# Kernel optimization log

Measured on AMD Instinct MI355X. Metric: run time of the kernel, lower is better.

Reference implementation:

```python
import jax, jax.numpy as jnp
import numpy as np

WL_W = 8   # weight quantization bits (args.wl_weight)
WL_A = 8   # activation quantization bits (args.wl_activate)
EPS = 1e-5


def _quant_ste(x, bits):
    """Symmetric per-tensor uniform quantization with straight-through estimator,
    emulating NeuroSim's wage-style weight/activation quantization in QConv2d."""
    n = float(2 ** (bits - 1) - 1)
    s = jnp.max(jnp.abs(x)) + 1e-12
    xq = jnp.round(x / s * n) / n * s
    return x + jax.lax.stop_gradient(xq - x)


def _qconv(x, w):
    # quantize input and weight, then 3x3 conv, stride 1, padding 1 (NCHW/OIHW)
    xq = _quant_ste(x, WL_A)
    wq = _quant_ste(w, WL_W)
    return jax.lax.conv_general_dilated(
        xq, wq, window_strides=(1, 1), padding=((1, 1), (1, 1)),
        dimension_numbers=('NCHW', 'OIHW', 'NCHW'))


def _bn(x, gamma, beta):
    # training-mode BatchNorm2d: batch statistics over (N, H, W)
    mean = jnp.mean(x, axis=(0, 2, 3), keepdims=True)
    var = jnp.var(x, axis=(0, 2, 3), keepdims=True)
    xn = (x - mean) * jax.lax.rsqrt(var + EPS)
    return xn * gamma[None, :, None, None] + beta[None, :, None, None]


def setup_inputs() -> dict:
    key = jax.random.key(0)
    ks = jax.random.split(key, 3)
    B, C, H, W = 32, 128, 56, 56
    return {
        'x': jax.random.normal(ks[0], (B, C, H, W), dtype=jnp.float32),
        'w1': jax.random.normal(ks[1], (C, C, 3, 3), dtype=jnp.float32) * 0.05,
        'gamma1': jnp.ones((C,), dtype=jnp.float32),
        'beta1': jnp.zeros((C,), dtype=jnp.float32),
        'w2': jax.random.normal(ks[2], (C, C, 3, 3), dtype=jnp.float32) * 0.05,
        'gamma2': jnp.ones((C,), dtype=jnp.float32),
        'beta2': jnp.zeros((C,), dtype=jnp.float32),
    }


def reference(x, w1, gamma1, beta1, w2, gamma2, beta2):
    identity = x  # no downsample
    out = _qconv(x, w1)
    out = _bn(out, gamma1, beta1)
    out = jax.nn.relu(out)
    out = _qconv(out, w2)
    out = _bn(out, gamma2, beta2)
    out = out + identity
    return jax.nn.relu(out)
```

## Files before the change

### kernel.cpp

```cpp
#include <hip/hip_runtime.h>

#define NB 32
#define C 128
#define H 56
#define W 56
#define HWSZ (H*W)
#define ELTS (NB*C*HWSZ)
#define NHW (NB*HWSZ)
#define HP 59
#define SLAB 8192
#define GCONVX 28
#define NBLK (GCONVX*NB)
#define PSTRIDE (C*NBLK)

typedef __attribute__((ext_vector_type(8))) short bf16x8;
typedef __attribute__((ext_vector_type(4))) short short4v;
typedef __attribute__((ext_vector_type(4))) float f32x4;
typedef __attribute__((ext_vector_type(4))) int i32x4;

#define SLOT_SX 0
#define SLOT_SW1 1
#define SLOT_SW2 2
#define SLOT_SA2 3
#define SUM1 8
#define SSQ1 136
#define MAXE1 264
#define MAXNEG1 392
#define SCALE1 520
#define SHIFT1 648
#define SUM2 776
#define SSQ2 904
#define MAXE2 1032
#define MAXNEG2 1160
#define SCALE2 1288
#define SHIFT2 1416

#define META_OFF 0ull
#define META_BYTES 8192ull
#define XQ_OFF 8192ull
#define XQ_BYTES ((unsigned long long)NB*HP*SLAB)
#define A2Q_OFF (XQ_OFF + XQ_BYTES)
#define Y1_OFF (A2Q_OFF + XQ_BYTES)
#define Y_BYTES ((unsigned long long)ELTS*2ull)
#define Y2_OFF (Y1_OFF + Y_BYTES)
#define W1Q_OFF (Y2_OFF + Y_BYTES)
#define WQ_BYTES (9ull*2*128*64)
#define W2Q_OFF (W1Q_OFF + WQ_BYTES)
#define PART_OFF (W2Q_OFF + WQ_BYTES)
#define PART_BYTES (4ull*PSTRIDE*4ull)

__device__ __forceinline__ short f2bf_rne(float f) {
    unsigned u = __float_as_uint(f);
    return (short)((u + 0x7FFFu + ((u >> 16) & 1u)) >> 16);
}
__device__ __forceinline__ float bf2f(short s) {
    return __uint_as_float(((unsigned)(unsigned short)s) << 16);
}

__global__ void absmax_kernel(const float* __restrict__ p, int n4, unsigned* __restrict__ slot) {
    __shared__ float red[256];
    float m = 0.f;
    int stride = gridDim.x * blockDim.x;
    for (int i = blockIdx.x * blockDim.x + threadIdx.x; i < n4; i += stride) {
        f32x4 v = ((const f32x4*)p)[i];
        m = fmaxf(m, fmaxf(fmaxf(fabsf(v.x), fabsf(v.y)), fmaxf(fabsf(v.z), fabsf(v.w))));
    }
    red[threadIdx.x] = m;
    __syncthreads();
    for (int s = 128; s > 0; s >>= 1) {
        if (threadIdx.x < s) red[threadIdx.x] = fmaxf(red[threadIdx.x], red[threadIdx.x + s]);
        __syncthreads();
    }
    if (threadIdx.x == 0) atomicMax(slot, __float_as_uint(red[0]));
}

__global__ void pad_zero_kernel(char* __restrict__ xq, char* __restrict__ a2q) {
    int hp = blockIdx.x;
    int n = blockIdx.y;
    char* base = (blockIdx.z ? a2q : xq) + ((size_t)n * HP + hp) * SLAB;
    int t = threadIdx.x;
    if (hp == 0 || hp >= 57) {
        f32x4 z = {0.f, 0.f, 0.f, 0.f};
        *(f32x4*)(base + t * 16) = z;
        *(f32x4*)(base + 4096 + t * 16) = z;
    } else {
        if (t < 32) *(int*)(base + t * 4) = 0;
        else        *(int*)(base + 7296 + (t - 32) * 4) = 0;
    }
}

__global__ void quant_w_kernel(const float* __restrict__ w, const float* __restrict__ meta,
                               int slot, char* __restrict__ wq) {
    int idx = blockIdx.x * 256 + threadIdx.x;
    int co = idx >> 7, ci = idx & 127;
    float qs = 127.f / (meta[slot] + 1e-12f);
    const float* src = w + ((size_t)(co * 128 + ci)) * 9;
    int cc = ci >> 6, cl = ci & 63;
    #pragma unroll
    for (int tap = 0; tap < 9; ++tap) {
        int q = (int)rintf(src[tap] * qs);
        wq[(((size_t)tap * 2 + cc) * 128 + co) * 64 + cl] = (char)q;
    }
}

__global__ void quant_x_kernel(const float* __restrict__ x, const float* __restrict__ meta,
                               char* __restrict__ xq) {
    __shared__ float tile[128][57];
    int h = blockIdx.x, n = blockIdx.y, t = threadIdx.x;
    int ci = t >> 1, seg = (t & 1) * 28;
    const float* row = x + (((size_t)(n * C + ci)) * H + h) * W + seg;
    #pragma unroll
    for (int j = 0; j < 28; j += 4) {
        f32x4 v = *(const f32x4*)(row + j);
        tile[ci][seg + j + 0] = v.x;
        tile[ci][seg + j + 1] = v.y;
        tile[ci][seg + j + 2] = v.z;
        tile[ci][seg + j + 3] = v.w;
    }
    __syncthreads();
    float qs = 127.f / (meta[SLOT_SX] + 1e-12f);
    int w = t & 63, cq = t >> 6;
    if (w < 56) {
        char* slab = xq + ((size_t)n * HP + (h + 1)) * SLAB;
        int wp = w + 1;
        #pragma unroll
        for (int c2 = 0; c2 < 2; ++c2) {
            union { char c[16]; i32x4 v; } u;
            #pragma unroll
            for (int j = 0; j < 16; ++j)
                u.c[j] = (char)(int)rintf(tile[cq * 32 + c2 * 16 + j][w] * qs);
            int L = wp * 128 + cq * 32 + c2 * 16;
            *(i32x4*)(slab + (L ^ ((wp & 7) << 4))) = u.v;
        }
    }
}

__global__ __launch_bounds__(256, 4) void conv_mfma_kernel(
        const char* __restrict__ xq, const char* __restrict__ wq,
        short* __restrict__ y, const float* __restrict__ meta,
        float* __restrict__ part, int slot_in, int slot_w) {
    __shared__ __align__(16) char lds[4 * SLAB + 512];
    const int n = blockIdx.y, h0 = blockIdx.x * 2;
    const int t = threadIdx.x, lane = t & 63;
    const int co0 = (t >> 6) * 32, l15 = lane & 15, lg = lane >> 4;

    const char* slabbase = xq + ((size_t)n * HP + h0) * SLAB;
    #pragma unroll
    for (int s = 0; s < 4; ++s) {
        #pragma unroll
        for (int i = 0; i < 2; ++i) {
            int off = (i * 256 + t) * 16;
            __builtin_amdgcn_global_load_lds(
                (const __attribute__((address_space(1))) unsigned*)(slabbase + s * SLAB + off),
                (__attribute__((address_space(3))) unsigned*)(lds + s * SLAB + off), 16, 0, 0);
        }
    }

    i32x4 acc[2][4][2] = {};

    #pragma unroll
    for (int kh = 0; kh < 3; ++kh) {
        if (kh == 0)      { asm volatile("s_waitcnt vmcnt(4)" ::: "memory"); }
        else if (kh == 1) { asm volatile("s_waitcnt vmcnt(2)" ::: "memory"); }
        else              { asm volatile("s_waitcnt vmcnt(0)" ::: "memory"); }
        __builtin_amdgcn_s_barrier();
        #pragma unroll
        for (int kw = 0; kw < 3; ++kw) {
            #pragma unroll
            for (int cc = 0; cc < 2; ++cc) {
                const char* wt = wq + (((kh * 3 + kw) * 2 + cc) << 13);
                i32x4 a0 = *(const i32x4*)(wt + (co0 + l15) * 64 + lg * 16);
                i32x4 a1 = *(const i32x4*)(wt + (co0 + 16 + l15) * 64 + lg * 16);
                #pragma unroll
                for (int r = 0; r < 2; ++r) {
                    const char* Bb = lds + (kh + r) * SLAB;
                    #pragma unroll
                    for (int fj = 0; fj < 4; ++fj) {
                        int wpp = fj * 16 + l15 + kw;
                        int L = (wpp << 7) + (cc << 6) + (lg << 4);
                        i32x4 b = *(const i32x4*)(Bb + (L ^ ((wpp & 7) << 4)));
                        acc[r][fj][0] = __builtin_amdgcn_mfma_i32_16x16x64_i8(a0, b, acc[r][fj][0], 0, 0, 0);
                        acc[r][fj][1] = __builtin_amdgcn_mfma_i32_16x16x64_i8(a1, b, acc[r][fj][1], 0, 0, 0);
                    }
                }
            }
        }
    }

    float dq = (meta[slot_in] + 1e-12f) * (meta[slot_w] + 1e-12f) * (1.f / 16129.f);

    float a_sum[8] = {}, a_ssq[8] = {}, a_mx[8], a_mxn[8];
    #pragma unroll
    for (int i = 0; i < 8; ++i) { a_mx[i] = -1e30f; a_mxn[i] = -1e30f; }

    #pragma unroll
    for (int r = 0; r < 2; ++r) {
        short* yrow = y + (((size_t)n * H + (h0 + r)) * W) * C;
        #pragma unroll
        for (int ai = 0; ai < 2; ++ai) {
            #pragma unroll
            for (int fj = 0; fj < 4; ++fj) {
                int wo = fj * 16 + l15;
                if (wo < W) {
                    short4v pk;
                    #pragma unroll
                    for (int q = 0; q < 4; ++q) {
                        float v = (float)acc[r][fj][ai][q] * dq;
                        int si = ai * 4 + q;
                        a_sum[si] += v;
                        a_ssq[si] += v * v;
                        a_mx[si]  = fmaxf(a_mx[si], v);
                        a_mxn[si] = fmaxf(a_mxn[si], -v);
                        pk[q] = f2bf_rne(v);
                    }
                    *(short4v*)(yrow + (size_t)wo * C + co0 + ai * 16 + lg * 4) = pk;
                }
            }
        }
    }

    int bid = blockIdx.y * GCONVX + blockIdx.x;
    #pragma unroll
    for (int si = 0; si < 8; ++si) {
        float s1 = a_sum[si], s2 = a_ssq[si], m1 = a_mx[si], m2 = a_mxn[si];
        #pragma unroll
        for (int m = 1; m < 16; m <<= 1) {
            s1 += __shfl_xor(s1, m, 64);
            s2 += __shfl_xor(s2, m, 64);
            m1 = fmaxf(m1, __shfl_xor(m1, m, 64));
            m2 = fmaxf(m2, __shfl_xor(m2, m, 64));
        }
        if (l15 == 0) {
            int cch = co0 + (si >> 2) * 16 + lg * 4 + (si & 3);
            part[0 * PSTRIDE + cch * NBLK + bid] = s1;
            part[1 * PSTRIDE + cch * NBLK + bid] = s2;
            part[2 * PSTRIDE + cch * NBLK + bid] = m1;
            part[3 * PSTRIDE + cch * NBLK + bid] = m2;
        }
    }
}

__global__ void bn_reduce_kernel(const float* __restrict__ part, float* __restrict__ meta,
                                 int sum_off, int ssq_off, int maxe_off, int maxneg_off) {
    __shared__ float r1[256], r2[256], r3[256], r4[256];
    int c = blockIdx.x, t = threadIdx.x;
    const float* ps = part + 0 * PSTRIDE + (size_t)c * NBLK;
    const float* pq = part + 1 * PSTRIDE + (size_t)c * NBLK;
    const float* pm = part + 2 * PSTRIDE + (size_t)c * NBLK;
    const float* pn = part + 3 * PSTRIDE + (size_t)c * NBLK;
    float s1 = 0.f, s2 = 0.f, m1 = -1e30f, m2 = -1e30f;
    for (int i = t; i < NBLK; i += 256) {
        s1 += ps[i];
        s2 += pq[i];
        m1 = fmaxf(m1, pm[i]);
        m2 = fmaxf(m2, pn[i]);
    }
    r1[t] = s1; r2[t] = s2; r3[t] = m1; r4[t] = m2;
    __syncthreads();
    for (int k = 128; k > 0; k >>= 1) {
        if (t < k) {
            r1[t] += r1[t + k];
            r2[t] += r2[t + k];
            r3[t] = fmaxf(r3[t], r3[t + k]);
            r4[t] = fmaxf(r4[t], r4[t + k]);
        }
        __syncthreads();
    }
    if (t == 0) {
        meta[sum_off + c] = r1[0];
        meta[ssq_off + c] = r2[0];
        meta[maxe_off + c] = r3[0];
        meta[maxneg_off + c] = r4[0];
    }
}

__global__ void bn_finalize_kernel(float* __restrict__ meta, int sum_off, int ssq_off,
                                   int maxe_off, int maxneg_off, int scale_off, int shift_off,
                                   int amax_slot,
                                   const float* __restrict__ gamma, const float* __restrict__ beta) {
    __shared__ float red[128];
    int c = threadIdx.x;
    float mean = meta[sum_off + c] * (1.f / NHW);
    float var = meta[ssq_off + c] * (1.f / NHW) - mean * mean;
    float istd = rsqrtf(var + 1e-5f);
    float sc = gamma[c] * istd;
    float sh = beta[c] - mean * sc;
    meta[scale_off + c] = sc;
    meta[shift_off + c] = sh;
    if (amax_slot >= 0) {
        float vmax = meta[maxe_off + c];
        float vmin = -meta[maxneg_off + c];
        float cand = fmaxf(0.f, fmaxf(sc * vmax + sh, sc * vmin + sh));
        red[c] = cand;
        __syncthreads();
        for (int k = 64; k > 0; k >>= 1) {
            if (c < k) red[c] = fmaxf(red[c], red[c + k]);
            __syncthreads();
        }
        if (c == 0) meta[amax_slot] = red[0];
    }
}

__global__ void quant_bnrelu_kernel(const short* __restrict__ y1, const float* __restrict__ meta,
                                    char* __restrict__ a2q) {
    int h = blockIdx.x, n = blockIdx.y, t = threadIdx.x;
    const short* row = y1 + (((size_t)n * H + h) * W) * C;
    float qs = 127.f / (meta[SLOT_SA2] + 1e-12f);
    char* slab = a2q + ((size_t)n * HP + (h + 1)) * SLAB;
    #pragma unroll
    for (int i = 0; i < 2; ++i) {
        int g = i * 256 + t;
        if (g < 448) {
            int w = g >> 3, cg = g & 7;
            bf16x8 v0 = *(const bf16x8*)(row + w * 128 + cg * 16);
            bf16x8 v1 = *(const bf16x8*)(row + w * 128 + cg * 16 + 8);
            union { char c[16]; i32x4 v; } u;
            #pragma unroll
            for (int j = 0; j < 8; ++j) {
                float a = fmaxf(bf2f(v0[j]) * meta[SCALE1 + cg * 16 + j] + meta[SHIFT1 + cg * 16 + j], 0.f);
                u.c[j] = (char)(int)rintf(a * qs);
            }
            #pragma unroll
            for (int j = 0; j < 8; ++j) {
                float a = fmaxf(bf2f(v1[j]) * meta[SCALE1 + cg * 16 + 8 + j] + meta[SHIFT1 + cg * 16 + 8 + j], 0.f);
                u.c[8 + j] = (char)(int)rintf(a * qs);
            }
            int wp = w + 1;
            int L = wp * 128 + cg * 16;
            *(i32x4*)(slab + (L ^ ((wp & 7) << 4))) = u.v;
        }
    }
}

__global__ void final_kernel(const short* __restrict__ y2, const float* __restrict__ x,
                             const float* __restrict__ meta, float* __restrict__ out) {
    __shared__ short tile[56 * 128];
    int h = blockIdx.x, n = blockIdx.y, t = threadIdx.x;
    const short* row = y2 + (((size_t)n * H + h) * W) * C;
    #pragma unroll
    for (int i = 0; i < 4; ++i) {
        int g = i * 256 + t;
        if (g < 896) *(bf16x8*)(tile + g * 8) = *(const bf16x8*)(row + g * 8);
    }
    __syncthreads();
    int c = t >> 1, seg = (t & 1) * 28;
    float sc = meta[SCALE2 + c], sh = meta[SHIFT2 + c];
    const float* xr = x + (((size_t)(n * C + c)) * H + h) * W + seg;
    float* orow = out + (((size_t)(n * C + c)) * H + h) * W + seg;
    #pragma unroll
    for (int j = 0; j < 28; j += 4) {
        f32x4 xv = *(const f32x4*)(xr + j);
        f32x4 o;
        #pragma unroll
        for (int k = 0; k < 4; ++k) {
            float yv = bf2f(tile[(seg + j + k) * 128 + c]);
            o[k] = fmaxf(yv * sc + sh + xv[k], 0.f);
        }
        *(f32x4*)(orow + j) = o;
    }
}

extern "C" void kernel_launch(void* const* d_in, const int* in_sizes, int n_in,
                              void* d_out, int out_size, void* d_ws, size_t ws_size,
                              hipStream_t stream) {
    const float* x      = (const float*)d_in[0];
    const float* w1     = (const float*)d_in[1];
    const float* gamma1 = (const float*)d_in[2];
    const float* beta1  = (const float*)d_in[3];
    const float* w2     = (const float*)d_in[4];
    const float* gamma2 = (const float*)d_in[5];
    const float* beta2  = (const float*)d_in[6];
    float* out = (float*)d_out;
    char* ws = (char*)d_ws;

    float* meta = (float*)(ws + META_OFF);
    unsigned* metau = (unsigned*)meta;
    char* xq   = ws + XQ_OFF;
    char* a2q  = ws + A2Q_OFF;
    short* y1  = (short*)(ws + Y1_OFF);
    short* y2  = (short*)(ws + Y2_OFF);
    char* w1q  = ws + W1Q_OFF;
    char* w2q  = ws + W2Q_OFF;
    float* part = (float*)(ws + PART_OFF);

    hipMemsetAsync(ws + META_OFF, 0, META_BYTES, stream);
    pad_zero_kernel<<<dim3(59, 32, 2), 256, 0, stream>>>(xq, a2q);

    absmax_kernel<<<1024, 256, 0, stream>>>(x, ELTS / 4, metau + SLOT_SX);
    absmax_kernel<<<64, 256, 0, stream>>>(w1, 147456 / 4, metau + SLOT_SW1);
    absmax_kernel<<<64, 256, 0, stream>>>(w2, 147456 / 4, metau + SLOT_SW2);

    quant_w_kernel<<<64, 256, 0, stream>>>(w1, meta, SLOT_SW1, w1q);
    quant_w_kernel<<<64, 256, 0, stream>>>(w2, meta, SLOT_SW2, w2q);

    dim3 ghn(56, 32);
    quant_x_kernel<<<ghn, 256, 0, stream>>>(x, meta, xq);

    dim3 gconv(GCONVX, 32);
    conv_mfma_kernel<<<gconv, 256, 0, stream>>>(xq, w1q, y1, meta, part, SLOT_SX, SLOT_SW1);
    bn_reduce_kernel<<<128, 256, 0, stream>>>(part, meta, SUM1, SSQ1, MAXE1, MAXNEG1);
    bn_finalize_kernel<<<1, 128, 0, stream>>>(meta, SUM1, SSQ1, MAXE1, MAXNEG1,
                                              SCALE1, SHIFT1, SLOT_SA2, gamma1, beta1);
    quant_bnrelu_kernel<<<ghn, 256, 0, stream>>>(y1, meta, a2q);

    conv_mfma_kernel<<<gconv, 256, 0, stream>>>(a2q, w2q, y2, meta, part, SLOT_SA2, SLOT_SW2);
    bn_reduce_kernel<<<128, 256, 0, stream>>>(part, meta, SUM2, SSQ2, MAXE2, MAXNEG2);
    bn_finalize_kernel<<<1, 128, 0, stream>>>(meta, SUM2, SSQ2, MAXE2, MAXNEG2,
                                              SCALE2, SHIFT2, -1, gamma2, beta2);

    final_kernel<<<ghn, 256, 0, stream>>>(y2, x, meta, out);
}
```

Before: 251.3 us.

## Fuse small kernels and remap conv waves to row-by-channel-half tiles

Several small launches are merged. The meta memset moves into pad_zero, the two weight absmax and quant launches become single 2-D grids, and bn_finalize is folded into bn_reduce, which now publishes the activation absmax with an atomicMax. The conv kernel also changes its wave mapping: each wave now computes one output row for 64 output channels (four A fragments per B load) instead of two rows for 32 channels. This roughly halves the LDS B reads per MFMA but doubles the global weight-fragment loads, and the partial-statistics array doubles in size. The goal is to cut launch overhead and LDS traffic, at the cost of more weight reads and register pressure.

```diff
diff --git a/kernel.cpp b/kernel.cpp
--- a/kernel.cpp
+++ b/kernel.cpp
@@ -11,7 +11,8 @@
 #define SLAB 8192
 #define GCONVX 28
 #define NBLK (GCONVX*NB)
-#define PSTRIDE (C*NBLK)
+#define NBLK2 (NBLK*2)
+#define PSTRIDE2 (C*NBLK2)
 
 typedef __attribute__((ext_vector_type(8))) short bf16x8;
 typedef __attribute__((ext_vector_type(4))) short short4v;
@@ -22,18 +23,10 @@
 #define SLOT_SW1 1
 #define SLOT_SW2 2
 #define SLOT_SA2 3
-#define SUM1 8
-#define SSQ1 136
-#define MAXE1 264
-#define MAXNEG1 392
-#define SCALE1 520
-#define SHIFT1 648
-#define SUM2 776
-#define SSQ2 904
-#define MAXE2 1032
-#define MAXNEG2 1160
-#define SCALE2 1288
-#define SHIFT2 1416
+#define SCALE1 8
+#define SHIFT1 136
+#define SCALE2 264
+#define SHIFT2 392
 
 #define META_OFF 0ull
 #define META_BYTES 8192ull
@@ -47,7 +40,7 @@
 #define WQ_BYTES (9ull*2*128*64)
 #define W2Q_OFF (W1Q_OFF + WQ_BYTES)
 #define PART_OFF (W2Q_OFF + WQ_BYTES)
-#define PART_BYTES (4ull*PSTRIDE*4ull)
+#define PART_BYTES (4ull*PSTRIDE2*4ull)
 
 __device__ __forceinline__ short f2bf_rne(float f) {
     unsigned u = __float_as_uint(f);
@@ -74,11 +67,37 @@
     if (threadIdx.x == 0) atomicMax(slot, __float_as_uint(red[0]));
 }
 
-__global__ void pad_zero_kernel(char* __restrict__ xq, char* __restrict__ a2q) {
+__global__ void absmax_w_kernel(const float* __restrict__ w1, const float* __restrict__ w2,
+                                unsigned* __restrict__ metau) {
+    __shared__ float red[256];
+    const float* p = blockIdx.y ? w2 : w1;
+    unsigned* slot = metau + (blockIdx.y ? SLOT_SW2 : SLOT_SW1);
+    const int n4 = 147456 / 4;
+    float m = 0.f;
+    int stride = gridDim.x * blockDim.x;
+    for (int i = blockIdx.x * blockDim.x + threadIdx.x; i < n4; i += stride) {
+        f32x4 v = ((const f32x4*)p)[i];
+        m = fmaxf(m, fmaxf(fmaxf(fabsf(v.x), fabsf(v.y)), fmaxf(fabsf(v.z), fabsf(v.w))));
+    }
+    red[threadIdx.x] = m;
+    __syncthreads();
+    for (int s = 128; s > 0; s >>= 1) {
+        if (threadIdx.x < s) red[threadIdx.x] = fmaxf(red[threadIdx.x], red[threadIdx.x + s]);
+        __syncthreads();
+    }
+    if (threadIdx.x == 0) atomicMax(slot, __float_as_uint(red[0]));
+}
+
+__global__ void pad_zero_kernel(char* __restrict__ xq, char* __restrict__ a2q,
+                                float* __restrict__ meta) {
     int hp = blockIdx.x;
     int n = blockIdx.y;
     char* base = (blockIdx.z ? a2q : xq) + ((size_t)n * HP + hp) * SLAB;
     int t = threadIdx.x;
+    if (blockIdx.z == 0 && blockIdx.x == 0 && blockIdx.y == 0) {
+        #pragma unroll
+        for (int j = 0; j < 8; ++j) meta[j * 256 + t] = 0.f;
+    }
     if (hp == 0 || hp >= 57) {
         f32x4 z = {0.f, 0.f, 0.f, 0.f};
         *(f32x4*)(base + t * 16) = z;
@@ -89,11 +108,14 @@
     }
 }
 
-__global__ void quant_w_kernel(const float* __restrict__ w, const float* __restrict__ meta,
-                               int slot, char* __restrict__ wq) {
+__global__ void quant_w_kernel(const float* __restrict__ w1, const float* __restrict__ w2,
+                               const float* __restrict__ meta,
+                               char* __restrict__ w1q, char* __restrict__ w2q) {
+    const float* w = blockIdx.y ? w2 : w1;
+    char* wq = blockIdx.y ? w2q : w1q;
+    float qs = 127.f / (meta[blockIdx.y ? SLOT_SW2 : SLOT_SW1] + 1e-12f);
     int idx = blockIdx.x * 256 + threadIdx.x;
     int co = idx >> 7, ci = idx & 127;
-    float qs = 127.f / (meta[slot] + 1e-12f);
     const float* src = w + ((size_t)(co * 128 + ci)) * 9;
     int cc = ci >> 6, cl = ci & 63;
     #pragma unroll
@@ -142,7 +164,8 @@
     __shared__ __align__(16) char lds[4 * SLAB + 512];
     const int n = blockIdx.y, h0 = blockIdx.x * 2;
     const int t = threadIdx.x, lane = t & 63;
-    const int co0 = (t >> 6) * 32, l15 = lane & 15, lg = lane >> 4;
+    const int wv = t >> 6, r = wv >> 1, ch = (wv & 1) * 64;
+    const int l15 = lane & 15, lg = lane >> 4;
 
     const char* slabbase = xq + ((size_t)n * HP + h0) * SLAB;
     #pragma unroll
@@ -156,7 +179,7 @@
         }
     }
 
-    i32x4 acc[2][4][2] = {};
+    i32x4 acc[4][4] = {};
 
     #pragma unroll
     for (int kh = 0; kh < 3; ++kh) {
@@ -164,92 +187,89 @@
         else if (kh == 1) { asm volatile("s_waitcnt vmcnt(2)" ::: "memory"); }
         else              { asm volatile("s_waitcnt vmcnt(0)" ::: "memory"); }
         __builtin_amdgcn_s_barrier();
+        const char* Bb = lds + (kh + r) * SLAB;
         #pragma unroll
         for (int kw = 0; kw < 3; ++kw) {
             #pragma unroll
             for (int cc = 0; cc < 2; ++cc) {
                 const char* wt = wq + (((kh * 3 + kw) * 2 + cc) << 13);
-                i32x4 a0 = *(const i32x4*)(wt + (co0 + l15) * 64 + lg * 16);
-                i32x4 a1 = *(const i32x4*)(wt + (co0 + 16 + l15) * 64 + lg * 16);
+                i32x4 a[4];
                 #pragma unroll
-                for (int r = 0; r < 2; ++r) {
-                    const char* Bb = lds + (kh + r) * SLAB;
+                for (int ct = 0; ct < 4; ++ct)
+                    a[ct] = *(const i32x4*)(wt + (ch + ct * 16 + l15) * 64 + lg * 16);
+                #pragma unroll
+                for (int fj = 0; fj < 4; ++fj) {
+                    int wpp = fj * 16 + l15 + kw;
+                    int L = (wpp << 7) + (cc << 6) + (lg << 4);
+                    i32x4 b = *(const i32x4*)(Bb + (L ^ ((wpp & 7) << 4)));
                     #pragma unroll
-                    for (int fj = 0; fj < 4; ++fj) {
-                        int wpp = fj * 16 + l15 + kw;
-                        int L = (wpp << 7) + (cc << 6) + (lg << 4);
-                        i32x4 b = *(const i32x4*)(Bb + (L ^ ((wpp & 7) << 4)));
-                        acc[r][fj][0] = __builtin_amdgcn_mfma_i32_16x16x64_i8(a0, b, acc[r][fj][0], 0, 0, 0);
-                        acc[r][fj][1] = __builtin_amdgcn_mfma_i32_16x16x64_i8(a1, b, acc[r][fj][1], 0, 0, 0);
-                    }
+                    for (int ct = 0; ct < 4; ++ct)
+                        acc[ct][fj] = __builtin_amdgcn_mfma_i32_16x16x64_i8(a[ct], b, acc[ct][fj], 0, 0, 0);
                 }
             }
         }
     }
 
     float dq = (meta[slot_in] + 1e-12f) * (meta[slot_w] + 1e-12f) * (1.f / 16129.f);
-
-    float a_sum[8] = {}, a_ssq[8] = {}, a_mx[8], a_mxn[8];
-    #pragma unroll
-    for (int i = 0; i < 8; ++i) { a_mx[i] = -1e30f; a_mxn[i] = -1e30f; }
-
-    #pragma unroll
-    for (int r = 0; r < 2; ++r) {
-        short* yrow = y + (((size_t)n * H + (h0 + r)) * W) * C;
-        #pragma unroll
-        for (int ai = 0; ai < 2; ++ai) {
-            #pragma unroll
-            for (int fj = 0; fj < 4; ++fj) {
-                int wo = fj * 16 + l15;
-                if (wo < W) {
-                    short4v pk;
-                    #pragma unroll
-                    for (int q = 0; q < 4; ++q) {
-                        float v = (float)acc[r][fj][ai][q] * dq;
-                        int si = ai * 4 + q;
-                        a_sum[si] += v;
-                        a_ssq[si] += v * v;
-                        a_mx[si]  = fmaxf(a_mx[si], v);
-                        a_mxn[si] = fmaxf(a_mxn[si], -v);
-                        pk[q] = f2bf_rne(v);
-                    }
-                    *(short4v*)(yrow + (size_t)wo * C + co0 + ai * 16 + lg * 4) = pk;
+    short* yrow = y + (((size_t)n * H + (h0 + r)) * W) * C;
+    int bcol = (blockIdx.y * GCONVX + blockIdx.x) * 2 + r;
+
+    #pragma unroll
+    for (int ct = 0; ct < 4; ++ct) {
+        float s1[4] = {}, s2[4] = {}, m1[4], m2[4];
+        #pragma unroll
+        for (int q = 0; q < 4; ++q) { m1[q] = -1e30f; m2[q] = -1e30f; }
+        #pragma unroll
+        for (int fj = 0; fj < 4; ++fj) {
+            int wo = fj * 16 + l15;
+            if (wo < W) {
+                short4v pk;
+                #pragma unroll
+                for (int q = 0; q < 4; ++q) {
+                    float v = (float)acc[ct][fj][q] * dq;
+                    s1[q] += v;
+                    s2[q] += v * v;
+                    m1[q] = fmaxf(m1[q], v);
+                    m2[q] = fmaxf(m2[q], -v);
+                    pk[q] = f2bf_rne(v);
                 }
-            }
-        }
-    }
-
-    int bid = blockIdx.y * GCONVX + blockIdx.x;
-    #pragma unroll
-    for (int si = 0; si < 8; ++si) {
-        float s1 = a_sum[si], s2 = a_ssq[si], m1 = a_mx[si], m2 = a_mxn[si];
-        #pragma unroll
-        for (int m = 1; m < 16; m <<= 1) {
-            s1 += __shfl_xor(s1, m, 64);
-            s2 += __shfl_xor(s2, m, 64);
-            m1 = fmaxf(m1, __shfl_xor(m1, m, 64));
-            m2 = fmaxf(m2, __shfl_xor(m2, m, 64));
+                *(short4v*)(yrow + (size_t)wo * C + ch + ct * 16 + lg * 4) = pk;
+            }
+        }
+        #pragma unroll
+        for (int q = 0; q < 4; ++q) {
+            #pragma unroll
+            for (int m = 1; m < 16; m <<= 1) {
+                s1[q] += __shfl_xor(s1[q], m, 64);
+                s2[q] += __shfl_xor(s2[q], m, 64);
+                m1[q] = fmaxf(m1[q], __shfl_xor(m1[q], m, 64));
+                m2[q] = fmaxf(m2[q], __shfl_xor(m2[q], m, 64));
+            }
         }
         if (l15 == 0) {
-            int cch = co0 + (si >> 2) * 16 + lg * 4 + (si & 3);
-            part[0 * PSTRIDE + cch * NBLK + bid] = s1;
-            part[1 * PSTRIDE + cch * NBLK + bid] = s2;
-            part[2 * PSTRIDE + cch * NBLK + bid] = m1;
-            part[3 * PSTRIDE + cch * NBLK + bid] = m2;
+            #pragma unroll
+            for (int q = 0; q < 4; ++q) {
+                int cch = ch + ct * 16 + lg * 4 + q;
+                part[0 * PSTRIDE2 + (size_t)cch * NBLK2 + bcol] = s1[q];
+                part[1 * PSTRIDE2 + (size_t)cch * NBLK2 + bcol] = s2[q];
+                part[2 * PSTRIDE2 + (size_t)cch * NBLK2 + bcol] = m1[q];
+                part[3 * PSTRIDE2 + (size_t)cch * NBLK2 + bcol] = m2[q];
+            }
         }
     }
 }
 
 __global__ void bn_reduce_kernel(const float* __restrict__ part, float* __restrict__ meta,
-                                 int sum_off, int ssq_off, int maxe_off, int maxneg_off) {
+                                 const float* __restrict__ gamma, const float* __restrict__ beta,
+                                 int scale_off, int shift_off, int amax_slot) {
     __shared__ float r1[256], r2[256], r3[256], r4[256];
     int c = blockIdx.x, t = threadIdx.x;
-    const float* ps = part + 0 * PSTRIDE + (size_t)c * NBLK;
-    const float* pq = part + 1 * PSTRIDE + (size_t)c * NBLK;
-    const float* pm = part + 2 * PSTRIDE + (size_t)c * NBLK;
-    const float* pn = part + 3 * PSTRIDE + (size_t)c * NBLK;
+    const float* ps = part + 0 * PSTRIDE2 + (size_t)c * NBLK2;
+    const float* pq = part + 1 * PSTRIDE2 + (size_t)c * NBLK2;
+    const float* pm = part + 2 * PSTRIDE2 + (size_t)c * NBLK2;
+    const float* pn = part + 3 * PSTRIDE2 + (size_t)c * NBLK2;
     float s1 = 0.f, s2 = 0.f, m1 = -1e30f, m2 = -1e30f;
-    for (int i = t; i < NBLK; i += 256) {
+    for (int i = t; i < NBLK2; i += 256) {
         s1 += ps[i];
         s2 += pq[i];
         m1 = fmaxf(m1, pm[i]);
@@ -267,37 +287,17 @@
         __syncthreads();
     }
     if (t == 0) {
-        meta[sum_off + c] = r1[0];
-        meta[ssq_off + c] = r2[0];
-        meta[maxe_off + c] = r3[0];
-        meta[maxneg_off + c] = r4[0];
-    }
-}
-
-__global__ void bn_finalize_kernel(float* __restrict__ meta, int sum_off, int ssq_off,
-                                   int maxe_off, int maxneg_off, int scale_off, int shift_off,
-                                   int amax_slot,
-                                   const float* __restrict__ gamma, const float* __restrict__ beta) {
-    __shared__ float red[128];
-    int c = threadIdx.x;
-    float mean = meta[sum_off + c] * (1.f / NHW);
-    float var = meta[ssq_off + c] * (1.f / NHW) - mean * mean;
-    float istd = rsqrtf(var + 1e-5f);
-    float sc = gamma[c] * istd;
-    float sh = beta[c] - mean * sc;
-    meta[scale_off + c] = sc;
-    meta[shift_off + c] = sh;
-    if (amax_slot >= 0) {
-        float vmax = meta[maxe_off + c];
-        float vmin = -meta[maxneg_off + c];
-        float cand = fmaxf(0.f, fmaxf(sc * vmax + sh, sc * vmin + sh));
-        red[c] = cand;
-        __syncthreads();
-        for (int k = 64; k > 0; k >>= 1) {
-            if (c < k) red[c] = fmaxf(red[c], red[c + k]);
-            __syncthreads();
-        }
-        if (c == 0) meta[amax_slot] = red[0];
+        float mean = r1[0] * (1.f / NHW);
+        float var = r2[0] * (1.f / NHW) - mean * mean;
+        float istd = rsqrtf(var + 1e-5f);
+        float sc = gamma[c] * istd;
+        float sh = beta[c] - mean * sc;
+        meta[scale_off + c] = sc;
+        meta[shift_off + c] = sh;
+        if (amax_slot >= 0) {
+            float cand = fmaxf(0.f, fmaxf(sc * r3[0] + sh, sc * (-r4[0]) + sh));
+            atomicMax((unsigned*)meta + amax_slot, __float_as_uint(cand));
+        }
     }
 }
 
@@ -383,30 +383,22 @@
     char* w2q  = ws + W2Q_OFF;
     float* part = (float*)(ws + PART_OFF);
 
-    hipMemsetAsync(ws + META_OFF, 0, META_BYTES, stream);
-    pad_zero_kernel<<<dim3(59, 32, 2), 256, 0, stream>>>(xq, a2q);
+    pad_zero_kernel<<<dim3(59, 32, 2), 256, 0, stream>>>(xq, a2q, meta);
 
     absmax_kernel<<<1024, 256, 0, stream>>>(x, ELTS / 4, metau + SLOT_SX);
-    absmax_kernel<<<64, 256, 0, stream>>>(w1, 147456 / 4, metau + SLOT_SW1);
-    absmax_kernel<<<64, 256, 0, stream>>>(w2, 147456 / 4, metau + SLOT_SW2);
-
-    quant_w_kernel<<<64, 256, 0, stream>>>(w1, meta, SLOT_SW1, w1q);
-    quant_w_kernel<<<64, 256, 0, stream>>>(w2, meta, SLOT_SW2, w2q);
+    absmax_w_kernel<<<dim3(64, 2), 256, 0, stream>>>(w1, w2, metau);
+    quant_w_kernel<<<dim3(64, 2), 256, 0, stream>>>(w1, w2, meta, w1q, w2q);
 
     dim3 ghn(56, 32);
     quant_x_kernel<<<ghn, 256, 0, stream>>>(x, meta, xq);
 
     dim3 gconv(GCONVX, 32);
     conv_mfma_kernel<<<gconv, 256, 0, stream>>>(xq, w1q, y1, meta, part, SLOT_SX, SLOT_SW1);
-    bn_reduce_kernel<<<128, 256, 0, stream>>>(part, meta, SUM1, SSQ1, MAXE1, MAXNEG1);
-    bn_finalize_kernel<<<1, 128, 0, stream>>>(meta, SUM1, SSQ1, MAXE1, MAXNEG1,
-                                              SCALE1, SHIFT1, SLOT_SA2, gamma1, beta1);
+    bn_reduce_kernel<<<128, 256, 0, stream>>>(part, meta, gamma1, beta1, SCALE1, SHIFT1, SLOT_SA2);
     quant_bnrelu_kernel<<<ghn, 256, 0, stream>>>(y1, meta, a2q);
 
     conv_mfma_kernel<<<gconv, 256, 0, stream>>>(a2q, w2q, y2, meta, part, SLOT_SA2, SLOT_SW2);
-    bn_reduce_kernel<<<128, 256, 0, stream>>>(part, meta, SUM2, SSQ2, MAXE2, MAXNEG2);
-    bn_finalize_kernel<<<1, 128, 0, stream>>>(meta, SUM2, SSQ2, MAXE2, MAXNEG2,
-                                              SCALE2, SHIFT2, -1, gamma2, beta2);
+    bn_reduce_kernel<<<128, 256, 0, stream>>>(part, meta, gamma2, beta2, SCALE2, SHIFT2, -1);
 
     final_kernel<<<ghn, 256, 0, stream>>>(y2, x, meta, out);
 }
```

Result: slower. 266.0 us (+5.8%).
